# Performance work log

Hardware: AMD Instinct MI355X
Metric: run time of the kernel (lower is better)

Reference implementation:

```python
import jax, jax.numpy as jnp
import numpy as np
import math

B, S, E, H = 4096, 10, 1536, 12
HD = E // H
SCALE = HD ** -0.5
LN_EPS = 1e-5


def make_pe(d_model=E, max_len=S):
    pos = np.arange(max_len, dtype=np.float32)[:, None]
    div = np.exp(np.arange(0, d_model, 2, dtype=np.float32) * (-math.log(10000.0) / d_model))
    pe = np.zeros((max_len, d_model), dtype=np.float32)
    pe[:, 0::2] = np.sin(pos * div)
    pe[:, 1::2] = np.cos(pos * div)
    return jnp.asarray(pe)


def setup_inputs() -> dict:
    key = jax.random.key(0)
    ks = jax.random.split(key, 10)
    inp = {
        "a_vectors": jax.random.normal(ks[0], (B, S, E), jnp.float32),
        "b_vectors": jax.random.normal(ks[1], (B, S, E), jnp.float32),
    }
    # prefix-valid masks: True = padding (as the torch module expects)
    len_a = jax.random.randint(ks[2], (B,), 1, S + 1)
    len_b = jax.random.randint(ks[3], (B,), 1, S + 1)
    pos = jnp.arange(S)
    inp["mask_a"] = pos[None, :] >= len_a[:, None]
    inp["mask_b"] = pos[None, :] >= len_b[:, None]
    # learned params: weights stored [in, out]; y = x @ W + b
    for i, name in enumerate(["q", "k", "v", "o", "f"]):
        kw = jax.random.fold_in(ks[4], i)
        inp[name + "_w"] = jax.random.normal(kw, (E, E), jnp.float32) * (E ** -0.5)
        inp[name + "_b"] = jnp.zeros((E,), jnp.float32)
    inp["ln_g"] = jnp.ones((E,), jnp.float32)
    inp["ln_b"] = jnp.zeros((E,), jnp.float32)
    return inp


def _layernorm(x, g, b):
    mu = jnp.mean(x, axis=-1, keepdims=True)
    var = jnp.mean((x - mu) ** 2, axis=-1, keepdims=True)
    return (x - mu) * jax.lax.rsqrt(var + LN_EPS) * g + b


def _branch(x, mask, q_w, q_b, k_w, k_b, v_w, v_b, o_w, o_b, f_w, f_b, ln_g, ln_b, pe):
    # dropout is identity (eval mode)
    x = _layernorm(x + pe[None, :, :], ln_g, ln_b)          # [B,S,E]
    # gather last valid vector (prefix-valid mask)
    last_idx = jnp.sum(~mask, axis=1) - 1                    # [B]
    last = jnp.take_along_axis(x, last_idx[:, None, None], axis=1)[:, 0, :]  # [B,E]
    q = (last @ q_w + q_b).reshape(B, H, HD)                 # [B,H,HD]
    k = (x @ k_w + k_b).reshape(B, S, H, HD)                 # [B,S,H,HD]
    v = (x @ v_w + v_b).reshape(B, S, H, HD)
    scores = jnp.einsum("bhd,bshd->bhs", q, k) * SCALE       # [B,H,S]
    scores = jnp.where(mask[:, None, :], -1e9, scores)
    w = jax.nn.softmax(scores, axis=-1)
    ctx = jnp.einsum("bhs,bshd->bhd", w, v).reshape(B, E)    # [B,E]
    out = ctx @ o_w + o_b
    return jax.nn.gelu(out @ f_w + f_b, approximate=False)   # [B,E]


def reference(a_vectors, b_vectors, mask_a, mask_b,
              q_w, q_b, k_w, k_b, v_w, v_b, o_w, o_b, f_w, f_b, ln_g, ln_b):
    pe = make_pe()
    params = (q_w, q_b, k_w, k_b, v_w, v_b, o_w, o_b, f_w, f_b, ln_g, ln_b, pe)
    a_rep = _branch(a_vectors, mask_a, *params)
    b_rep = _branch(b_vectors, mask_b, *params)
    return (a_rep, b_rep)
```

## Files before the change

### kernel.cpp

```cpp
#include <hip/hip_runtime.h>
#include <math.h>

#define BB 4096
#define SS 10
#define EE 1536
#define HH 12
#define HDIM 128
#define MROWS (BB * SS)
#define BB2 (2 * BB)
#define MROWS2 (2 * MROWS)

typedef short short8 __attribute__((ext_vector_type(8)));
typedef float f32x4 __attribute__((ext_vector_type(4)));
typedef const unsigned char __attribute__((address_space(1))) gu8;
typedef unsigned char __attribute__((address_space(3))) lu8;

__device__ __forceinline__ unsigned short f2bf(float x) {
  unsigned int u = __float_as_uint(x);
  return (unsigned short)((u + 0x7FFFu + ((u >> 16) & 1u)) >> 16);
}
__device__ __forceinline__ float bf2f(unsigned short u) {
  return __uint_as_float(((unsigned int)u) << 16);
}

__global__ void k_detect(const unsigned int* __restrict__ m, int* __restrict__ flags) {
  int lb = 0, lf = 0;
  int stride = gridDim.x * blockDim.x;
  for (int i = blockIdx.x * blockDim.x + threadIdx.x; i < BB * SS / 4; i += stride) {
    unsigned int wv = m[i];
    if ((wv >> 8) & 0xFFu) lb = 1;
    if (wv >> 16) lf = 1;
  }
  if (lb) atomicOr(&flags[0], 1);
  if (lf) atomicOr(&flags[1], 1);
}

__global__ void k_lastidx(const void* __restrict__ ma, const void* __restrict__ mb,
                          const int* __restrict__ flags, int* __restrict__ lastidx) {
  int idx = blockIdx.x * blockDim.x + threadIdx.x;
  if (idx >= BB2) return;
  const void* m = (idx >= BB) ? mb : ma;
  int b = idx & (BB - 1);
  int f = flags[0] ? 1 : (flags[1] ? 2 : 0);
  int len = 0;
  for (int s = 0; s < SS; ++s) {
    int j = b * SS + s;
    int pad;
    if (f == 1)      pad = ((const unsigned char*)m)[j] != 0;
    else if (f == 2) pad = ((const float*)m)[j] != 0.0f;
    else             pad = ((const int*)m)[j] != 0;
    len += (pad == 0);
  }
  lastidx[idx] = len - 1;
}

__global__ void k_pe(float* __restrict__ pe) {
  int idx = blockIdx.x * blockDim.x + threadIdx.x;
  if (idx >= SS * EE) return;
  int s = idx / EE, e = idx - (idx / EE) * EE;
  float fe = (float)(e & ~1);
  float freq = expf(fe * (-9.210340371976184f / (float)EE));
  float arg = (float)s * freq;
  pe[idx] = (e & 1) ? cosf(arg) : sinf(arg);
}

__global__ void k_trans(const float* __restrict__ w0, const float* __restrict__ w1,
                        const float* __restrict__ w2, const float* __restrict__ w3,
                        const float* __restrict__ w4, unsigned short* __restrict__ wt) {
  __shared__ float tile[32][33];
  int z = blockIdx.z;
  const float* W = z == 0 ? w0 : z == 1 ? w1 : z == 2 ? w2 : z == 3 ? w3 : w4;
  unsigned short* T = wt + (size_t)z * EE * EE;
  int n0 = blockIdx.x * 32, k0 = blockIdx.y * 32;
  int tx = threadIdx.x, ty = threadIdx.y;
#pragma unroll
  for (int i = 0; i < 4; ++i)
    tile[ty + i * 8][tx] = W[(size_t)(k0 + ty + i * 8) * EE + n0 + tx];
  __syncthreads();
#pragma unroll
  for (int i = 0; i < 4; ++i)
    T[(size_t)(n0 + ty + i * 8) * EE + k0 + tx] = f2bf(tile[tx][ty + i * 8]);
}

__global__ void k_cast(const float* __restrict__ in, unsigned short* __restrict__ out) {
  int i = (blockIdx.x * blockDim.x + threadIdx.x) * 8;
  if (i >= EE * EE) return;
  float4 a = *(const float4*)(in + i);
  float4 b = *(const float4*)(in + i + 4);
  short8 v;
  v[0] = (short)f2bf(a.x); v[1] = (short)f2bf(a.y);
  v[2] = (short)f2bf(a.z); v[3] = (short)f2bf(a.w);
  v[4] = (short)f2bf(b.x); v[5] = (short)f2bf(b.y);
  v[6] = (short)f2bf(b.z); v[7] = (short)f2bf(b.w);
  *(short8*)(out + i) = v;
}

__global__ __launch_bounds__(256) void k_ln(
    const float* __restrict__ av, const float* __restrict__ bv,
    const float* __restrict__ pe,
    const float* __restrict__ g, const float* __restrict__ be,
    const int* __restrict__ lastidx,
    unsigned short* __restrict__ xln, unsigned short* __restrict__ lastx) {
  int w = threadIdx.x >> 6, lane = threadIdx.x & 63;
  int row = blockIdx.x * 4 + w;
  const float* xin = (row < MROWS) ? (av + (size_t)row * EE)
                                   : (bv + (size_t)(row - MROWS) * EE);
  int bg = row / SS, s = row - bg * SS;
  const float4* x4 = (const float4*)xin;
  const float4* p4 = (const float4*)(pe + s * EE);
  float4 v[6];
  float s1 = 0.f, s2 = 0.f;
#pragma unroll
  for (int j = 0; j < 6; ++j) {
    float4 a = x4[j * 64 + lane], p = p4[j * 64 + lane];
    a.x += p.x; a.y += p.y; a.z += p.z; a.w += p.w;
    v[j] = a;
    s1 += a.x + a.y + a.z + a.w;
    s2 += a.x * a.x + a.y * a.y + a.z * a.z + a.w * a.w;
  }
#pragma unroll
  for (int off = 32; off; off >>= 1) {
    s1 += __shfl_xor(s1, off, 64);
    s2 += __shfl_xor(s2, off, 64);
  }
  float mu = s1 * (1.0f / EE);
  float var = s2 * (1.0f / EE) - mu * mu;
  float scl = rsqrtf(var + 1e-5f);
  bool isLast = (s == lastidx[bg]);
  uint2* orow = (uint2*)(xln + (size_t)row * EE);
  uint2* lrow = (uint2*)(lastx + (size_t)bg * EE);
  const float4* g4 = (const float4*)g;
  const float4* b4 = (const float4*)be;
#pragma unroll
  for (int j = 0; j < 6; ++j) {
    int idx = j * 64 + lane;
    float4 gg = g4[idx], bb = b4[idx];
    float o0 = (v[j].x - mu) * scl * gg.x + bb.x;
    float o1 = (v[j].y - mu) * scl * gg.y + bb.y;
    float o2 = (v[j].z - mu) * scl * gg.z + bb.z;
    float o3 = (v[j].w - mu) * scl * gg.w + bb.w;
    uint2 pk;
    pk.x = (unsigned int)f2bf(o0) | ((unsigned int)f2bf(o1) << 16);
    pk.y = (unsigned int)f2bf(o2) | ((unsigned int)f2bf(o3) << 16);
    orow[idx] = pk;
    if (isLast) lrow[idx] = pk;
  }
}

__global__ __launch_bounds__(256) void k_gemm_g(
    const unsigned short* __restrict__ A, int aStrH, int lda,
    const unsigned short* __restrict__ Bt, int bStrH, int ldb,
    const float* __restrict__ bias, int biasStrH,
    void* __restrict__ C, int cStrH, int ldc,
    int MB, int NB, int K) {
  __shared__ __align__(16) unsigned char smA[8192];
  __shared__ __align__(16) unsigned char smB[8192];
  int h = blockIdx.y;
  const unsigned char* Ab = (const unsigned char*)(A + (size_t)h * aStrH);
  const unsigned char* Bb = (const unsigned char*)(Bt + (size_t)h * bStrH);
  const float* bi = bias ? bias + (size_t)h * biasStrH : nullptr;
  int per = MB >> 3;
  int bid = blockIdx.x;
  int xcd = bid & 7, lin = bid >> 3;
  int mt = xcd * per + lin / NB;
  int nt = lin % NB;
  int m0 = mt << 7, n0 = nt << 7;
  int tid = threadIdx.x, wid = tid >> 6, lane = tid & 63;
  int wm = wid >> 1, wn = wid & 1;
  f32x4 acc[4][4] = {};
  const size_t ldaB = (size_t)lda * 2, ldbB = (size_t)ldb * 2;
  int lrow = lane & 15, kgrp = lane >> 4;
  int aoff = (wm * 64 + lrow) * 64 + kgrp * 16;
  int boff = (wn * 64 + lrow) * 64 + kgrp * 16;
  int Lbase = wid * 1024 + lane * 16;
  const int nk = K >> 5;
  for (int kt = 0; kt < nk; ++kt) {
    int k0b = kt << 6;
#pragma unroll
    for (int issue = 0; issue < 2; ++issue) {
      int L = issue * 4096 + Lbase;
      int row = L >> 6, colb = L & 63;
      int Lu = issue * 4096 + wid * 1024;
      __builtin_amdgcn_global_load_lds((gu8*)(Ab + (size_t)(m0 + row) * ldaB + k0b + colb),
                                       (lu8*)(smA + Lu), 16, 0, 0);
      __builtin_amdgcn_global_load_lds((gu8*)(Bb + (size_t)(n0 + row) * ldbB + k0b + colb),
                                       (lu8*)(smB + Lu), 16, 0, 0);
    }
    __syncthreads();
    short8 af[4], bfr[4];
#pragma unroll
    for (int i = 0; i < 4; ++i) {
      af[i]  = *(const short8*)(smA + aoff + i * 1024);
      bfr[i] = *(const short8*)(smB + boff + i * 1024);
    }
#pragma unroll
    for (int mi = 0; mi < 4; ++mi)
#pragma unroll
      for (int ni = 0; ni < 4; ++ni)
        acc[mi][ni] = __builtin_amdgcn_mfma_f32_16x16x32_bf16(af[mi], bfr[ni], acc[mi][ni], 0, 0, 0);
    __syncthreads();
  }
  int rbase = m0 + wm * 64 + (lane >> 4) * 4;
  int cbase = n0 + wn * 64 + (lane & 15);
#pragma unroll
  for (int mi = 0; mi < 4; ++mi) {
#pragma unroll
    for (int ni = 0; ni < 4; ++ni) {
      int c = cbase + ni * 16;
      float bv = bi ? bi[c] : 0.f;
#pragma unroll
      for (int j = 0; j < 4; ++j) {
        int r = rbase + mi * 16 + j;
        float val = acc[mi][ni][j] + bv;
        ((unsigned short*)C)[(size_t)h * cStrH + (size_t)r * ldc + c] = f2bf(val);
      }
    }
  }
}

#define MMAQ(AR_, BR_, QM, QN)                                                  \
  do {                                                                          \
    _Pragma("unroll")                                                           \
    for (int mi_ = 0; mi_ < 4; ++mi_) {                                         \
      _Pragma("unroll")                                                         \
      for (int ni_ = 0; ni_ < 2; ++ni_) {                                       \
        acc[(QM)*4 + mi_][(QN)*2 + ni_] = __builtin_amdgcn_mfma_f32_16x16x32_bf16( \
            AR_[mi_][0], BR_[ni_][0], acc[(QM)*4 + mi_][(QN)*2 + ni_], 0, 0, 0);   \
        acc[(QM)*4 + mi_][(QN)*2 + ni_] = __builtin_amdgcn_mfma_f32_16x16x32_bf16( \
            AR_[mi_][1], BR_[ni_][1], acc[(QM)*4 + mi_][(QN)*2 + ni_], 0, 0, 0);   \
      }                                                                         \
    }                                                                           \
  } while (0)

#define PHASE_MID()                                      \
  do {                                                   \
    __builtin_amdgcn_s_barrier();                        \
    asm volatile("s_waitcnt lgkmcnt(0)" ::: "memory");   \
    __builtin_amdgcn_s_setprio(1);                       \
  } while (0)
#define PHASE_END()                                      \
  do {                                                   \
    __builtin_amdgcn_s_setprio(0);                       \
    __builtin_amdgcn_s_barrier();                        \
  } while (0)

template<int EPI>
__global__ __launch_bounds__(512, 2) void k_gemm256(
    const unsigned short* __restrict__ A, const unsigned short* __restrict__ Bt,
    const float* __restrict__ bias,
    void* __restrict__ C, int M, int N, int K) {
  __shared__ __align__(16) unsigned char lds[131072];
  const int NT = K >> 6;
  const int niters = NT >> 1;
  const int Ntiles = N >> 8;
  const int perx = (M >> 8) >> 3;
  const int MTG = 4;
  int bid = blockIdx.x;
  int xcd = bid & 7, lin = bid >> 3;
  int grp = lin / (MTG * Ntiles);
  int rem = lin - grp * (MTG * Ntiles);
  int nt = rem / MTG, mi_ = rem - nt * MTG;
  int mt = xcd * perx + grp * MTG + mi_;
  int m0 = mt << 8, n0 = nt << 8;
  int tid = threadIdx.x;
  int w = tid >> 6, lane = tid & 63;
  int wm = w >> 2, wn = w & 3;
  const size_t lda = (size_t)K * 2;
  const unsigned char* Ag = (const unsigned char*)A;
  const unsigned char* Bg = (const unsigned char*)Bt;

  unsigned char* A0 = lds;
  unsigned char* B0 = lds + 32768;
  unsigned char* A1 = lds + 65536;
  unsigned char* B1 = lds + 98304;

  int lrows = lane >> 3;
  int colswz = (((lane & 7) ^ (lrows & 7)) << 4);
  int rowA = w * 8;
  int rowB = (w >> 2) * 64 + (w & 3) * 8;

  auto stageA = [&](unsigned char* ldsA, int q, int kt) {
    int cb = kt * 128 + colswz;
#pragma unroll
    for (int i = 0; i < 2; ++i) {
      int tr = q * 64 + i * 128 + rowA;
      __builtin_amdgcn_global_load_lds(
          (gu8*)(Ag + (size_t)(m0 + tr + lrows) * lda + cb),
          (lu8*)(ldsA + tr * 128), 16, 0, 0);
    }
  };
  auto stageB = [&](unsigned char* ldsB, int q, int kt) {
    int cb = kt * 128 + colswz;
#pragma unroll
    for (int i = 0; i < 2; ++i) {
      int tr = q * 32 + i * 128 + rowB;
      __builtin_amdgcn_global_load_lds(
          (gu8*)(Bg + (size_t)(n0 + tr + lrows) * lda + cb),
          (lu8*)(ldsB + tr * 128), 16, 0, 0);
    }
  };

  int lrow = lane & 15, kgrp = lane >> 4, r7 = lane & 7;
  int s0 = ((kgrp ^ r7) << 4), s1 = (((kgrp | 4) ^ r7) << 4);
  int abase = (wm * 128 + lrow) * 128;
  int bbase = (wn * 64 + lrow) * 128;

  short8 ar[4][2], br0[2][2], br1[2][2];
  f32x4 acc[8][4];
#pragma unroll
  for (int i = 0; i < 8; ++i)
#pragma unroll
    for (int j = 0; j < 4; ++j) acc[i][j] = (f32x4)0.f;

  auto ldA = [&](unsigned char* ldsA, int qm) {
#pragma unroll
    for (int mi2 = 0; mi2 < 4; ++mi2) {
      ar[mi2][0] = *(const short8*)(ldsA + abase + qm * 8192 + mi2 * 2048 + s0);
      ar[mi2][1] = *(const short8*)(ldsA + abase + qm * 8192 + mi2 * 2048 + s1);
    }
  };
  auto ldB = [&](unsigned char* ldsB, int qn, short8 (&br)[2][2]) {
#pragma unroll
    for (int ni2 = 0; ni2 < 2; ++ni2) {
      br[ni2][0] = *(const short8*)(ldsB + bbase + qn * 4096 + ni2 * 2048 + s0);
      br[ni2][1] = *(const short8*)(ldsB + bbase + qn * 4096 + ni2 * 2048 + s1);
    }
  };

  stageA(A0, 0, 0); stageB(B0, 0, 0); stageA(A0, 1, 0); stageB(B0, 1, 0);
  stageA(A1, 0, 1); stageB(B1, 0, 1);
  asm volatile("s_waitcnt vmcnt(8)" ::: "memory");
  __builtin_amdgcn_s_barrier();

  for (int it = 0; it < niters - 1; ++it) {
    int t1 = 2 * it + 1, t2 = 2 * it + 2, t3 = 2 * it + 3;
    ldA(A0, 0); ldB(B0, 0, br0);
    stageA(A1, 1, t1);
    asm volatile("s_waitcnt vmcnt(6)" ::: "memory");
    PHASE_MID(); MMAQ(ar, br0, 0, 0); PHASE_END();
    ldB(B0, 1, br1);
    stageB(B1, 1, t1);
    PHASE_MID(); MMAQ(ar, br1, 0, 1); PHASE_END();
    ldA(A0, 1);
    stageA(A0, 0, t2);
    PHASE_MID(); MMAQ(ar, br0, 1, 0); PHASE_END();
    stageB(B0, 0, t2);
    asm volatile("s_waitcnt vmcnt(8)" ::: "memory");
    PHASE_MID(); MMAQ(ar, br1, 1, 1); PHASE_END();
    ldA(A1, 0); ldB(B1, 0, br0);
    stageA(A0, 1, t2);
    asm volatile("s_waitcnt vmcnt(6)" ::: "memory");
    PHASE_MID(); MMAQ(ar, br0, 0, 0); PHASE_END();
    ldB(B1, 1, br1);
    stageB(B0, 1, t2);
    PHASE_MID(); MMAQ(ar, br1, 0, 1); PHASE_END();
    ldA(A1, 1);
    if (t3 < NT) stageA(A1, 0, t3);
    PHASE_MID(); MMAQ(ar, br0, 1, 0); PHASE_END();
    if (t3 < NT) stageB(B1, 0, t3);
    asm volatile("s_waitcnt vmcnt(8)" ::: "memory");
    PHASE_MID(); MMAQ(ar, br1, 1, 1); PHASE_END();
  }
  {
    int t1 = NT - 1;
    ldA(A0, 0); ldB(B0, 0, br0);
    stageA(A1, 1, t1);
    asm volatile("s_waitcnt vmcnt(6)" ::: "memory");
    PHASE_MID(); MMAQ(ar, br0, 0, 0); PHASE_END();
    ldB(B0, 1, br1);
    stageB(B1, 1, t1);
    PHASE_MID(); MMAQ(ar, br1, 0, 1); PHASE_END();
    ldA(A0, 1);
    PHASE_MID(); MMAQ(ar, br0, 1, 0); PHASE_END();
    asm volatile("s_waitcnt vmcnt(4)" ::: "memory");
    PHASE_MID(); MMAQ(ar, br1, 1, 1); PHASE_END();
    ldA(A1, 0); ldB(B1, 0, br0);
    asm volatile("s_waitcnt vmcnt(2)" ::: "memory");
    PHASE_MID(); MMAQ(ar, br0, 0, 0); PHASE_END();
    ldB(B1, 1, br1);
    asm volatile("s_waitcnt vmcnt(0)" ::: "memory");
    PHASE_MID(); MMAQ(ar, br1, 0, 1); PHASE_END();
    ldA(A1, 1);
    PHASE_MID(); MMAQ(ar, br0, 1, 0); PHASE_END();
    PHASE_MID(); MMAQ(ar, br1, 1, 1); PHASE_END();
  }

  int rb = m0 + wm * 128 + (lane >> 4) * 4;
  int cb2 = n0 + wn * 64 + (lane & 15);
#pragma unroll
  for (int fm = 0; fm < 8; ++fm)
#pragma unroll
    for (int fn = 0; fn < 4; ++fn) {
      int c = cb2 + fn * 16;
      float bv = bias[c];
#pragma unroll
      for (int j = 0; j < 4; ++j) {
        int r = rb + fm * 16 + j;
        float val = acc[fm][fn][j] + bv;
        if (EPI == 2) {
          val = 0.5f * val * (1.0f + erff(val * 0.7071067811865476f));
          ((float*)C)[(size_t)r * N + c] = val;
        } else {
          ((unsigned short*)C)[(size_t)r * N + c] = f2bf(val);
        }
      }
    }
}

__global__ __launch_bounds__(256) void k_attn2(
    const unsigned short* __restrict__ xln,
    unsigned short* qky,
    const int* __restrict__ lastidx) {
  __shared__ __align__(16) unsigned short xs[10 * 1544];
  __shared__ float swp[4 * 256];
  __shared__ float wsm[120];
  int b = (BB2 - 1) - blockIdx.x;
  int t = threadIdx.x;
  const unsigned short* xg = xln + (size_t)b * SS * EE;
  unsigned short* qg = qky + (size_t)b * HH * EE;
#pragma unroll
  for (int j = 0; j < 8; ++j) {
    int idx = t + j * 256;
    if (idx < 1920) {
      int row = idx / 192, col = (idx - row * 192) * 8;
      *(short8*)(xs + row * 1544 + col) = *(const short8*)(xg + row * 1536 + col);
    }
  }
  __syncthreads();
  int w = t >> 6, lane = t & 63;
  int li = lastidx[b];
  {
    int hr = lane & 15; if (hr > 11) hr = 11;
    int sr = lane & 15; if (sr > 9) sr = 9;
    int kg = lane >> 4;
    f32x4 pacc = (f32x4)0.f;
#pragma unroll 4
    for (int kt = 0; kt < 12; ++kt) {
      int k0 = w * 384 + kt * 32 + kg * 8;
      short8 a  = *(const short8*)(qg + hr * 1536 + k0);
      short8 bf = *(const short8*)(xs + sr * 1544 + k0);
      pacc = __builtin_amdgcn_mfma_f32_16x16x32_bf16(a, bf, pacc, 0, 0, 0);
    }
    int prow = (lane >> 4) * 4, pcol = lane & 15;
#pragma unroll
    for (int j = 0; j < 4; ++j)
      swp[w * 256 + (prow + j) * 16 + pcol] = pacc[j];
  }
  __syncthreads();
  if (t < 120) {
    int h = t / 10, s = t - (t / 10) * 10;
    float v = swp[h * 16 + s] + swp[256 + h * 16 + s] +
              swp[512 + h * 16 + s] + swp[768 + h * 16 + s];
    wsm[t] = v * 0.08838834764831845f;
  }
  __syncthreads();
  if (t < 12) {
    float mx = -1e30f;
    for (int s = 0; s <= li; ++s) mx = fmaxf(mx, wsm[t * 10 + s]);
    float sum = 0.f;
    float ex[SS];
    for (int s = 0; s <= li; ++s) {
      ex[s] = expf(wsm[t * 10 + s] - mx);
      sum += ex[s];
    }
    float inv = 1.0f / sum;
    for (int s = 0; s <= li; ++s) wsm[t * 10 + s] = ex[s] * inv;
  }
  __syncthreads();
  float wv[3][10];
#pragma unroll
  for (int hl = 0; hl < 3; ++hl)
#pragma unroll
    for (int s = 0; s < 10; ++s)
      wv[hl][s] = (s <= li) ? wsm[(3 * w + hl) * 10 + s] : 0.f;
#pragma unroll 2
  for (int pass = 0; pass < 12; ++pass) {
    int e0 = pass * 128 + lane * 2;
    unsigned int xr[10];
#pragma unroll
    for (int s = 0; s < 10; ++s)
      xr[s] = *(const unsigned int*)(xs + s * 1544 + e0);
    float acc[3][2] = {};
#pragma unroll
    for (int s = 0; s < 10; ++s) {
      float xlo = bf2f((unsigned short)(xr[s] & 0xffff));
      float xhi = bf2f((unsigned short)(xr[s] >> 16));
#pragma unroll
      for (int hl = 0; hl < 3; ++hl) {
        acc[hl][0] += wv[hl][s] * xlo;
        acc[hl][1] += wv[hl][s] * xhi;
      }
    }
#pragma unroll
    for (int hl = 0; hl < 3; ++hl) {
      unsigned int pk = (unsigned int)f2bf(acc[hl][0]) | ((unsigned int)f2bf(acc[hl][1]) << 16);
      *(unsigned int*)(qg + (3 * w + hl) * 1536 + e0) = pk;
    }
  }
}

extern "C" void kernel_launch(void* const* d_in, const int* in_sizes, int n_in,
                              void* d_out, int out_size, void* d_ws, size_t ws_size,
                              hipStream_t stream) {
  (void)in_sizes; (void)n_in; (void)out_size; (void)ws_size;
  const float* av  = (const float*)d_in[0];
  const float* bv  = (const float*)d_in[1];
  const void*  ma  = d_in[2];
  const void*  mb  = d_in[3];
  const float* qw  = (const float*)d_in[4];
  const float* qb  = (const float*)d_in[5];
  const float* kw  = (const float*)d_in[6];
  const float* kb  = (const float*)d_in[7];  (void)kb;
  const float* vw  = (const float*)d_in[8];
  const float* vbs = (const float*)d_in[9];
  const float* ow  = (const float*)d_in[10];
  const float* ob  = (const float*)d_in[11];
  const float* fw  = (const float*)d_in[12];
  const float* fbs = (const float*)d_in[13];
  const float* lng = (const float*)d_in[14];
  const float* lnb = (const float*)d_in[15];

  unsigned char* ws = (unsigned char*)d_ws;
  size_t off = 0;
  auto alloc = [&](size_t bytes) {
    size_t r = off; off = (off + bytes + 255) & ~(size_t)255; return (void*)(ws + r);
  };
  int* flags            = (int*)alloc(8);
  float* pe             = (float*)alloc((size_t)SS * EE * 4);
  unsigned short* wt    = (unsigned short*)alloc((size_t)5 * EE * EE * 2);
  unsigned short* kwb   = (unsigned short*)alloc((size_t)EE * EE * 2);
  int* lastidx          = (int*)alloc((size_t)BB2 * 4);
  unsigned short* xln   = (unsigned short*)alloc((size_t)MROWS2 * EE * 2);
  unsigned short* lastx = (unsigned short*)alloc((size_t)BB2 * EE * 2);
  unsigned short* qbuf  = (unsigned short*)alloc((size_t)BB2 * EE * 2);
  unsigned short* qky   = (unsigned short*)alloc((size_t)BB2 * HH * EE * 2);
  unsigned short* ctx   = (unsigned short*)alloc((size_t)BB2 * EE * 2);
  unsigned short* o1    = (unsigned short*)alloc((size_t)BB2 * EE * 2);

  unsigned short* wt_q = wt;
  unsigned short* wt_v = wt + (size_t)2 * EE * EE;
  unsigned short* wt_o = wt + (size_t)3 * EE * EE;
  unsigned short* wt_f = wt + (size_t)4 * EE * EE;

  hipMemsetAsync(flags, 0, 8, stream);
  k_detect<<<40, 256, 0, stream>>>((const unsigned int*)ma, flags);
  k_pe<<<(SS * EE + 255) / 256, 256, 0, stream>>>(pe);
  k_trans<<<dim3(EE / 32, EE / 32, 5), dim3(32, 8), 0, stream>>>(qw, kw, vw, ow, fw, wt);
  k_cast<<<(EE * EE / 8 + 255) / 256, 256, 0, stream>>>(kw, kwb);
  k_lastidx<<<(BB2 + 255) / 256, 256, 0, stream>>>(ma, mb, flags, lastidx);

  k_ln<<<MROWS2 / 4, 256, 0, stream>>>(av, bv, pe, lng, lnb, lastidx, xln, lastx);
  k_gemm256<0><<<(BB2 / 256) * (EE / 256), 512, 0, stream>>>(
      lastx, wt_q, qb, qbuf, BB2, EE, EE);
  k_gemm_g<<<dim3(64 * 12, HH), 256, 0, stream>>>(
      qbuf, HDIM, EE, kwb, HDIM, EE, nullptr, 0, qky, EE, HH * EE, 64, 12, HDIM);
  k_attn2<<<BB2, 256, 0, stream>>>(xln, qky, lastidx);
  k_gemm_g<<<dim3(64 * 1, HH), 256, 0, stream>>>(
      qky, EE, HH * EE, wt_v, (size_t)0 + HDIM * EE, EE, vbs, HDIM,
      ctx, HDIM, EE, 64, 1, EE);
  k_gemm256<0><<<(BB2 / 256) * (EE / 256), 512, 0, stream>>>(
      ctx, wt_o, ob, o1, BB2, EE, EE);
  k_gemm256<2><<<(BB2 / 256) * (EE / 256), 512, 0, stream>>>(
      o1, wt_f, fbs, d_out, BB2, EE, EE);
}
```

Measured before the change: 830.4 us.

## Widen attention kernel to 512 threads and fold K cast into transpose

The attention kernel now runs 8 waves per batch row instead of 4. The score MFMA K-reduction is split across 8 waves, with a compact partial-score buffer, and the weighted-sum passes are split between two wave halves, so each wave does half the work. The separate fp32-to-bf16 cast of the K weight becomes a sixth z-slice of the transpose kernel, which removes one launch. The aim is more parallelism per block and fewer launches, at the cost of a larger cross-wave reduction and possibly lower occupancy.

```diff
diff --git a/kernel.cpp b/kernel.cpp
--- a/kernel.cpp
+++ b/kernel.cpp
@@ -66,13 +66,22 @@
 
 __global__ void k_trans(const float* __restrict__ w0, const float* __restrict__ w1,
                         const float* __restrict__ w2, const float* __restrict__ w3,
-                        const float* __restrict__ w4, unsigned short* __restrict__ wt) {
+                        const float* __restrict__ w4, unsigned short* __restrict__ wt,
+                        unsigned short* __restrict__ kwb) {
   __shared__ float tile[32][33];
   int z = blockIdx.z;
+  int n0 = blockIdx.x * 32, k0 = blockIdx.y * 32;
+  int tx = threadIdx.x, ty = threadIdx.y;
+  if (z == 5) {
+#pragma unroll
+    for (int i = 0; i < 4; ++i) {
+      size_t idx = (size_t)(k0 + ty + i * 8) * EE + n0 + tx;
+      kwb[idx] = f2bf(w1[idx]);
+    }
+    return;
+  }
   const float* W = z == 0 ? w0 : z == 1 ? w1 : z == 2 ? w2 : z == 3 ? w3 : w4;
   unsigned short* T = wt + (size_t)z * EE * EE;
-  int n0 = blockIdx.x * 32, k0 = blockIdx.y * 32;
-  int tx = threadIdx.x, ty = threadIdx.y;
 #pragma unroll
   for (int i = 0; i < 4; ++i)
     tile[ty + i * 8][tx] = W[(size_t)(k0 + ty + i * 8) * EE + n0 + tx];
@@ -80,19 +89,6 @@
 #pragma unroll
   for (int i = 0; i < 4; ++i)
     T[(size_t)(n0 + ty + i * 8) * EE + k0 + tx] = f2bf(tile[tx][ty + i * 8]);
-}
-
-__global__ void k_cast(const float* __restrict__ in, unsigned short* __restrict__ out) {
-  int i = (blockIdx.x * blockDim.x + threadIdx.x) * 8;
-  if (i >= EE * EE) return;
-  float4 a = *(const float4*)(in + i);
-  float4 b = *(const float4*)(in + i + 4);
-  short8 v;
-  v[0] = (short)f2bf(a.x); v[1] = (short)f2bf(a.y);
-  v[2] = (short)f2bf(a.z); v[3] = (short)f2bf(a.w);
-  v[4] = (short)f2bf(b.x); v[5] = (short)f2bf(b.y);
-  v[6] = (short)f2bf(b.z); v[7] = (short)f2bf(b.w);
-  *(short8*)(out + i) = v;
 }
 
 __global__ __launch_bounds__(256) void k_ln(
@@ -407,20 +403,20 @@
     }
 }
 
-__global__ __launch_bounds__(256) void k_attn2(
+__global__ __launch_bounds__(512, 6) void k_attn2(
     const unsigned short* __restrict__ xln,
     unsigned short* qky,
     const int* __restrict__ lastidx) {
   __shared__ __align__(16) unsigned short xs[10 * 1544];
-  __shared__ float swp[4 * 256];
+  __shared__ float swp[8 * 120];
   __shared__ float wsm[120];
   int b = (BB2 - 1) - blockIdx.x;
   int t = threadIdx.x;
   const unsigned short* xg = xln + (size_t)b * SS * EE;
   unsigned short* qg = qky + (size_t)b * HH * EE;
 #pragma unroll
-  for (int j = 0; j < 8; ++j) {
-    int idx = t + j * 256;
+  for (int j = 0; j < 4; ++j) {
+    int idx = t + j * 512;
     if (idx < 1920) {
       int row = idx / 192, col = (idx - row * 192) * 8;
       *(short8*)(xs + row * 1544 + col) = *(const short8*)(xg + row * 1536 + col);
@@ -434,23 +430,26 @@
     int sr = lane & 15; if (sr > 9) sr = 9;
     int kg = lane >> 4;
     f32x4 pacc = (f32x4)0.f;
-#pragma unroll 4
-    for (int kt = 0; kt < 12; ++kt) {
-      int k0 = w * 384 + kt * 32 + kg * 8;
+#pragma unroll
+    for (int kt = 0; kt < 6; ++kt) {
+      int k0 = w * 192 + kt * 32 + kg * 8;
       short8 a  = *(const short8*)(qg + hr * 1536 + k0);
       short8 bf = *(const short8*)(xs + sr * 1544 + k0);
       pacc = __builtin_amdgcn_mfma_f32_16x16x32_bf16(a, bf, pacc, 0, 0, 0);
     }
     int prow = (lane >> 4) * 4, pcol = lane & 15;
 #pragma unroll
-    for (int j = 0; j < 4; ++j)
-      swp[w * 256 + (prow + j) * 16 + pcol] = pacc[j];
+    for (int j = 0; j < 4; ++j) {
+      int r = prow + j;
+      if (r < 12 && pcol < 10)
+        swp[w * 120 + r * 10 + pcol] = pacc[j];
+    }
   }
   __syncthreads();
   if (t < 120) {
-    int h = t / 10, s = t - (t / 10) * 10;
-    float v = swp[h * 16 + s] + swp[256 + h * 16 + s] +
-              swp[512 + h * 16 + s] + swp[768 + h * 16 + s];
+    float v = 0.f;
+#pragma unroll
+    for (int ww = 0; ww < 8; ++ww) v += swp[ww * 120 + t];
     wsm[t] = v * 0.08838834764831845f;
   }
   __syncthreads();
@@ -467,14 +466,16 @@
     for (int s = 0; s <= li; ++s) wsm[t * 10 + s] = ex[s] * inv;
   }
   __syncthreads();
+  int hw = w & 3, ph = w >> 2;
   float wv[3][10];
 #pragma unroll
   for (int hl = 0; hl < 3; ++hl)
 #pragma unroll
     for (int s = 0; s < 10; ++s)
-      wv[hl][s] = (s <= li) ? wsm[(3 * w + hl) * 10 + s] : 0.f;
+      wv[hl][s] = (s <= li) ? wsm[(3 * hw + hl) * 10 + s] : 0.f;
 #pragma unroll 2
-  for (int pass = 0; pass < 12; ++pass) {
+  for (int pp = 0; pp < 6; ++pp) {
+    int pass = ph * 6 + pp;
     int e0 = pass * 128 + lane * 2;
     unsigned int xr[10];
 #pragma unroll
@@ -494,7 +495,7 @@
 #pragma unroll
     for (int hl = 0; hl < 3; ++hl) {
       unsigned int pk = (unsigned int)f2bf(acc[hl][0]) | ((unsigned int)f2bf(acc[hl][1]) << 16);
-      *(unsigned int*)(qg + (3 * w + hl) * 1536 + e0) = pk;
+      *(unsigned int*)(qg + (3 * hw + hl) * 1536 + e0) = pk;
     }
   }
 }
@@ -545,8 +546,7 @@
   hipMemsetAsync(flags, 0, 8, stream);
   k_detect<<<40, 256, 0, stream>>>((const unsigned int*)ma, flags);
   k_pe<<<(SS * EE + 255) / 256, 256, 0, stream>>>(pe);
-  k_trans<<<dim3(EE / 32, EE / 32, 5), dim3(32, 8), 0, stream>>>(qw, kw, vw, ow, fw, wt);
-  k_cast<<<(EE * EE / 8 + 255) / 256, 256, 0, stream>>>(kw, kwb);
+  k_trans<<<dim3(EE / 32, EE / 32, 6), dim3(32, 8), 0, stream>>>(qw, kw, vw, ow, fw, wt, kwb);
   k_lastidx<<<(BB2 + 255) / 256, 256, 0, stream>>>(ma, mb, flags, lastidx);
 
   k_ln<<<MROWS2 / 4, 256, 0, stream>>>(av, bv, pe, lng, lnb, lastidx, xln, lastx);
@@ -554,7 +554,7 @@
       lastx, wt_q, qb, qbuf, BB2, EE, EE);
   k_gemm_g<<<dim3(64 * 12, HH), 256, 0, stream>>>(
       qbuf, HDIM, EE, kwb, HDIM, EE, nullptr, 0, qky, EE, HH * EE, 64, 12, HDIM);
-  k_attn2<<<BB2, 256, 0, stream>>>(xln, qky, lastidx);
+  k_attn2<<<BB2, 512, 0, stream>>>(xln, qky, lastidx);
   k_gemm_g<<<dim3(64 * 1, HH), 256, 0, stream>>>(
       qky, EE, HH * EE, wt_v, (size_t)0 + HDIM * EE, EE, vbs, HDIM,
       ctx, HDIM, EE, 64, 1, EE);
```

New measurement: 1.172 ms. +41.2%, slower.
